# Performance work log

Hardware: AMD Instinct MI355X
Metric: run time of the kernel (lower is better)

The kernel has to match this reference:

```python
import jax, jax.numpy as jnp
import numpy as np

N_NODES = 50000
N_EDGES = 800000
IN_DIM = 128
HIDDEN = 64
HEADS = 4
N_GRAPHS = 256
NEG_SLOPE = 0.2  # PyG GATConv default


def gat_conv(x, src, dst, W, a_src, a_dst, b):
    """PyG-style GATConv (concat=True), eval mode (no dropout).
    x: [N, F_in]; src/dst: [E] (self-loops already included);
    W: [H*C, F_in]; a_src/a_dst: [H, C]; b: [H*C].
    """
    N = x.shape[0]
    H, C = a_src.shape
    h = (x @ W.T).reshape(N, H, C)                      # [N, H, C]
    alo = (h * a_src[None]).sum(-1)                     # [N, H]
    ahi = (h * a_dst[None]).sum(-1)                     # [N, H]
    e = jax.nn.leaky_relu(alo[src] + ahi[dst], NEG_SLOPE)  # [E, H]
    # segment softmax over destination neighborhoods
    m = jax.ops.segment_max(e, dst, num_segments=N)     # [N, H]
    ex = jnp.exp(e - m[dst])
    denom = jax.ops.segment_sum(ex, dst, num_segments=N)
    alpha = ex / (denom[dst] + 1e-16)                   # [E, H]
    out = jax.ops.segment_sum(h[src] * alpha[:, :, None], dst, num_segments=N)
    return out.reshape(N, H * C) + b


def setup_inputs() -> dict:
    key = jax.random.key(0)
    ks = jax.random.split(key, 24)
    p = lambda k, s: (jax.random.normal(k, s, jnp.float32) * 0.1)
    x = jax.random.normal(ks[0], (N_NODES, IN_DIM), jnp.float32)
    edge_index = jax.random.randint(ks[1], (2, N_EDGES), 0, N_NODES, jnp.int64 if jax.config.jax_enable_x64 else jnp.int32)
    batch_idx = jnp.sort(jax.random.randint(ks[2], (N_NODES,), 0, N_GRAPHS))
    HC = HIDDEN * HEADS
    return {
        "x": x, "edge_index": edge_index, "batch_idx": batch_idx,
        "W1": p(ks[3], (HC, IN_DIM)), "as1": p(ks[4], (HEADS, HIDDEN)), "ad1": p(ks[5], (HEADS, HIDDEN)), "b1": jnp.zeros((HC,), jnp.float32),
        "W2": p(ks[6], (HC, HC)), "as2": p(ks[7], (HEADS, HIDDEN)), "ad2": p(ks[8], (HEADS, HIDDEN)), "b2": jnp.zeros((HC,), jnp.float32),
        "W3": p(ks[9], (HIDDEN, HC)), "as3": p(ks[10], (1, HIDDEN)), "ad3": p(ks[11], (1, HIDDEN)), "b3": jnp.zeros((HIDDEN,), jnp.float32),
        "Wc1": p(ks[12], (HIDDEN, HIDDEN)), "bc1": jnp.zeros((HIDDEN,), jnp.float32),
        "Wc2": p(ks[13], (1, HIDDEN)), "bc2": jnp.zeros((1,), jnp.float32),
        "Wr1": p(ks[14], (HIDDEN, HIDDEN)), "br1": jnp.zeros((HIDDEN,), jnp.float32),
        "Wr2": p(ks[15], (1, HIDDEN)), "br2": jnp.zeros((1,), jnp.float32),
    }


def reference(x, edge_index, batch_idx, W1, as1, ad1, b1, W2, as2, ad2, b2, W3, as3, ad3, b3, Wc1, bc1, Wc2, bc2, Wr1, br1, Wr2, br2):
    N = x.shape[0]
    loops = jnp.arange(N, dtype=edge_index.dtype)
    src = jnp.concatenate([edge_index[0], loops])  # add_self_loops=True (PyG default)
    dst = jnp.concatenate([edge_index[1], loops])
    h = jax.nn.elu(gat_conv(x, src, dst, W1, as1, ad1, b1))
    h = jax.nn.elu(gat_conv(h, src, dst, W2, as2, ad2, b2))
    h = jax.nn.elu(gat_conv(h, src, dst, W3, as3, ad3, b3))  # [N, HIDDEN]
    # global mean pool over graphs
    cnt = jax.ops.segment_sum(jnp.ones((N,), h.dtype), batch_idx, num_segments=N_GRAPHS)
    g = jax.ops.segment_sum(h, batch_idx, num_segments=N_GRAPHS) / jnp.maximum(cnt, 1.0)[:, None]
    cls_logit = (jax.nn.relu(g @ Wc1.T + bc1) @ Wc2.T + bc2).reshape(-1)
    reg_pred = (jax.nn.relu(g @ Wr1.T + br1) @ Wr2.T + br2).reshape(-1)
    return (cls_logit, reg_pred)
```

## Files before the change

### kernel.cpp

```cpp
#include <hip/hip_runtime.h>

#define N_NODES 50000
#define N_EDGES 800000
#define EP_EDGES (N_EDGES + N_NODES)
#define N_GRAPHS 256
#define NBLK_SCAN ((N_NODES + 255) / 256)

typedef unsigned short u16;
typedef __attribute__((ext_vector_type(8))) short s8v;
typedef __attribute__((ext_vector_type(4))) float f4v;

__device__ __forceinline__ u16 fb(float f) {
  unsigned u = __float_as_uint(f);
  return (u16)((u + 0x7fffu + ((u >> 16) & 1u)) >> 16);
}
__device__ __forceinline__ float bfl(unsigned p) {
  return __uint_as_float(p << 16);
}
__device__ __forceinline__ float bfh(unsigned p) {
  return __uint_as_float(p & 0xffff0000u);
}
__device__ __forceinline__ float bff(u16 s) {
  return __uint_as_float(((unsigned)s) << 16);
}

#define W_N1 32768
#define W_N2 (W_N1 + 65536)
#define W_N3 (W_N2 + 16384)
__global__ void f2bw(const float* __restrict__ w1, const float* __restrict__ w2,
                     const float* __restrict__ w3, u16* __restrict__ w1b,
                     u16* __restrict__ w2b, u16* __restrict__ w3b) {
  int i = blockIdx.x * 256 + threadIdx.x;
  if (i < W_N1) w1b[i] = fb(w1[i]);
  else if (i < W_N2) w2b[i - W_N1] = fb(w2[i - W_N1]);
  else if (i < W_N3) w3b[i - W_N2] = fb(w3[i - W_N2]);
}

__device__ __forceinline__ void score_epilogue(
    f4v (&acc)[4][4], const float* __restrict__ a_src,
    const float* __restrict__ a_dst, float* __restrict__ alo,
    float* __restrict__ ahi, int m0, int n0, int wi, int wj, int quad, int fr,
    int M) {
  const int head = (n0 + wj) >> 6;
  float as[4], ad[4];
#pragma unroll
  for (int j = 0; j < 4; ++j) {
    int col = n0 + wj + j * 16 + fr;
    as[j] = a_src[col];
    ad[j] = a_dst[col];
  }
#pragma unroll
  for (int i = 0; i < 4; ++i) {
#pragma unroll
    for (int r = 0; r < 4; ++r) {
      float s = 0.f, d = 0.f;
#pragma unroll
      for (int j = 0; j < 4; ++j) {
        s += acc[i][j][r] * as[j];
        d += acc[i][j][r] * ad[j];
      }
#pragma unroll
      for (int off = 8; off; off >>= 1) {
        s += __shfl_xor(s, off, 64);
        d += __shfl_xor(d, off, 64);
      }
      int row = m0 + wi + i * 16 + quad * 4 + r;
      if (fr == 0 && row < M) {
        alo[row * 4 + head] = s;
        ahi[row * 4 + head] = d;
      }
    }
  }
}

__global__ __launch_bounds__(256) void gemm128(
    const u16* __restrict__ A, const u16* __restrict__ W,
    u16* __restrict__ C, const float* __restrict__ a_src,
    const float* __restrict__ a_dst, float* __restrict__ alo,
    float* __restrict__ ahi, int M, int Nout, int K) {
  __shared__ u16 As[128][40];
  __shared__ u16 Bs[128][40];
  const int t = threadIdx.x;
  const int m0 = blockIdx.y * 128, n0 = blockIdx.x * 128;
  const int rq = t >> 2, q = t & 3;
  const int w = t >> 6, lane = t & 63;
  const int wi = (w & 1) * 64, wj = (w >> 1) * 64;
  const int quad = lane >> 4, fr = lane & 15;

  f4v acc[4][4] = {};
  for (int k0 = 0; k0 < K; k0 += 32) {
    uint4 av[2], bv[2];
#pragma unroll
    for (int g = 0; g < 2; ++g) {
      int r = rq + g * 64;
      int m = m0 + r;
      av[g] = (m < M) ? *(const uint4*)&A[(size_t)m * K + k0 + q * 8]
                      : make_uint4(0, 0, 0, 0);
      bv[g] = *(const uint4*)&W[(size_t)(n0 + r) * K + k0 + q * 8];
    }
    __syncthreads();
#pragma unroll
    for (int g = 0; g < 2; ++g) {
      *(uint4*)&As[rq + g * 64][q * 8] = av[g];
      *(uint4*)&Bs[rq + g * 64][q * 8] = bv[g];
    }
    __syncthreads();
    s8v af[4], bf_[4];
#pragma unroll
    for (int i = 0; i < 4; ++i) {
      af[i] = *(const s8v*)&As[wi + i * 16 + fr][quad * 8];
      bf_[i] = *(const s8v*)&Bs[wj + i * 16 + fr][quad * 8];
    }
#pragma unroll
    for (int i = 0; i < 4; ++i)
#pragma unroll
      for (int j = 0; j < 4; ++j)
        acc[i][j] =
            __builtin_amdgcn_mfma_f32_16x16x32_bf16(af[i], bf_[j], acc[i][j], 0, 0, 0);
  }
#pragma unroll
  for (int i = 0; i < 4; ++i) {
    int rbase = m0 + wi + i * 16 + quad * 4;
#pragma unroll
    for (int j = 0; j < 4; ++j) {
      int col = n0 + wj + j * 16 + fr;
#pragma unroll
      for (int r = 0; r < 4; ++r) {
        int row = rbase + r;
        if (row < M) C[(size_t)row * Nout + col] = fb(acc[i][j][r]);
      }
    }
  }
  score_epilogue(acc, a_src, a_dst, alo, ahi, m0, n0, wi, wj, quad, fr, M);
}

__global__ __launch_bounds__(256) void gemm128_f32(
    const float* __restrict__ A, const u16* __restrict__ W,
    u16* __restrict__ C, const float* __restrict__ a_src,
    const float* __restrict__ a_dst, float* __restrict__ alo,
    float* __restrict__ ahi, int M, int Nout, int K) {
  __shared__ u16 As[128][40];
  __shared__ u16 Bs[128][40];
  const int t = threadIdx.x;
  const int m0 = blockIdx.y * 128, n0 = blockIdx.x * 128;
  const int rq = t >> 2, q = t & 3;
  const int w = t >> 6, lane = t & 63;
  const int wi = (w & 1) * 64, wj = (w >> 1) * 64;
  const int quad = lane >> 4, fr = lane & 15;

  f4v acc[4][4] = {};
  for (int k0 = 0; k0 < K; k0 += 32) {
    uint4 av[2], bv[2];
#pragma unroll
    for (int g = 0; g < 2; ++g) {
      int r = rq + g * 64;
      int m = m0 + r;
      if (m < M) {
        float4 f0 = *(const float4*)&A[(size_t)m * K + k0 + q * 8];
        float4 f1 = *(const float4*)&A[(size_t)m * K + k0 + q * 8 + 4];
        av[g].x = (unsigned)fb(f0.x) | ((unsigned)fb(f0.y) << 16);
        av[g].y = (unsigned)fb(f0.z) | ((unsigned)fb(f0.w) << 16);
        av[g].z = (unsigned)fb(f1.x) | ((unsigned)fb(f1.y) << 16);
        av[g].w = (unsigned)fb(f1.z) | ((unsigned)fb(f1.w) << 16);
      } else {
        av[g] = make_uint4(0, 0, 0, 0);
      }
      bv[g] = *(const uint4*)&W[(size_t)(n0 + r) * K + k0 + q * 8];
    }
    __syncthreads();
#pragma unroll
    for (int g = 0; g < 2; ++g) {
      *(uint4*)&As[rq + g * 64][q * 8] = av[g];
      *(uint4*)&Bs[rq + g * 64][q * 8] = bv[g];
    }
    __syncthreads();
    s8v af[4], bf_[4];
#pragma unroll
    for (int i = 0; i < 4; ++i) {
      af[i] = *(const s8v*)&As[wi + i * 16 + fr][quad * 8];
      bf_[i] = *(const s8v*)&Bs[wj + i * 16 + fr][quad * 8];
    }
#pragma unroll
    for (int i = 0; i < 4; ++i)
#pragma unroll
      for (int j = 0; j < 4; ++j)
        acc[i][j] =
            __builtin_amdgcn_mfma_f32_16x16x32_bf16(af[i], bf_[j], acc[i][j], 0, 0, 0);
  }
#pragma unroll
  for (int i = 0; i < 4; ++i) {
    int rbase = m0 + wi + i * 16 + quad * 4;
#pragma unroll
    for (int j = 0; j < 4; ++j) {
      int col = n0 + wj + j * 16 + fr;
#pragma unroll
      for (int r = 0; r < 4; ++r) {
        int row = rbase + r;
        if (row < M) C[(size_t)row * Nout + col] = fb(acc[i][j][r]);
      }
    }
  }
  score_epilogue(acc, a_src, a_dst, alo, ahi, m0, n0, wi, wj, quad, fr, M);
}

__global__ __launch_bounds__(256) void gemm_bf16(
    const u16* __restrict__ A, const u16* __restrict__ W,
    u16* __restrict__ C, int M, int Nout, int K) {
  __shared__ u16 As[64][40];
  __shared__ u16 Bs[64][40];
  const int t = threadIdx.x;
  const int m0 = blockIdx.y * 64, n0 = blockIdx.x * 64;
  const int r = t >> 2, c = t & 3;
  const int w = t >> 6, lane = t & 63;
  const int mi = (w & 1) * 32, ni = (w >> 1) * 32;
  const int quad = lane >> 4, fr = lane & 15;

  f4v c00{}, c01{}, c10{}, c11{};
  for (int k0 = 0; k0 < K; k0 += 32) {
    uint4 av = make_uint4(0, 0, 0, 0);
    int m = m0 + r;
    if (m < M) av = *(const uint4*)&A[(size_t)m * K + k0 + c * 8];
    uint4 bv = *(const uint4*)&W[(size_t)(n0 + r) * K + k0 + c * 8];
    __syncthreads();
    *(uint4*)&As[r][c * 8] = av;
    *(uint4*)&Bs[r][c * 8] = bv;
    __syncthreads();
    s8v a0 = *(const s8v*)&As[mi + fr][quad * 8];
    s8v a1 = *(const s8v*)&As[mi + 16 + fr][quad * 8];
    s8v b0 = *(const s8v*)&Bs[ni + fr][quad * 8];
    s8v b1 = *(const s8v*)&Bs[ni + 16 + fr][quad * 8];
    c00 = __builtin_amdgcn_mfma_f32_16x16x32_bf16(a0, b0, c00, 0, 0, 0);
    c01 = __builtin_amdgcn_mfma_f32_16x16x32_bf16(a0, b1, c01, 0, 0, 0);
    c10 = __builtin_amdgcn_mfma_f32_16x16x32_bf16(a1, b0, c10, 0, 0, 0);
    c11 = __builtin_amdgcn_mfma_f32_16x16x32_bf16(a1, b1, c11, 0, 0, 0);
  }
  const int col = n0 + ni + fr;
#pragma unroll
  for (int i = 0; i < 4; ++i) {
    int row = m0 + mi + quad * 4 + i;
    if (row < M) {
      C[(size_t)row * Nout + col] = fb(c00[i]);
      C[(size_t)row * Nout + col + 16] = fb(c01[i]);
    }
    int row2 = row + 16;
    if (row2 < M) {
      C[(size_t)row2 * Nout + col] = fb(c10[i]);
      C[(size_t)row2 * Nout + col + 16] = fb(c11[i]);
    }
  }
}

__global__ void k_hist(const int* __restrict__ ei, int* __restrict__ deg) {
  int e = blockIdx.x * 256 + threadIdx.x;
  if (e >= EP_EDGES) return;
  int d = (e < N_EDGES) ? ei[N_EDGES + e] : e - N_EDGES;
  atomicAdd(&deg[d], 1);
}

__global__ void k_scan_local(const int* __restrict__ deg,
                             int* __restrict__ rowstart,
                             int* __restrict__ bsum) {
  __shared__ int sh[256];
  const int tid = threadIdx.x;
  const int i = blockIdx.x * 256 + tid;
  int v = (i < N_NODES) ? deg[i] : 0;
  sh[tid] = v;
  __syncthreads();
  for (int off = 1; off < 256; off <<= 1) {
    int add = (tid >= off) ? sh[tid - off] : 0;
    __syncthreads();
    sh[tid] += add;
    __syncthreads();
  }
  if (i < N_NODES) rowstart[i] = sh[tid] - v;
  if (tid == 255) bsum[blockIdx.x] = sh[255];
}

__global__ void k_scan_bsum(int* __restrict__ bsum, int* __restrict__ boff) {
  __shared__ int sh[256];
  const int tid = threadIdx.x;
  int v = (tid < NBLK_SCAN) ? bsum[tid] : 0;
  sh[tid] = v;
  __syncthreads();
  for (int off = 1; off < 256; off <<= 1) {
    int add = (tid >= off) ? sh[tid - off] : 0;
    __syncthreads();
    sh[tid] += add;
    __syncthreads();
  }
  boff[tid] = sh[tid] - v;
}

__global__ void k_scan_add(int* __restrict__ rowstart,
                           const int* __restrict__ boff) {
  int i = blockIdx.x * 256 + threadIdx.x;
  if (i < N_NODES) rowstart[i] += boff[i >> 8];
  if (i == N_NODES) rowstart[N_NODES] = EP_EDGES;
}

__global__ void k_scatter(const int* __restrict__ ei,
                          const int* __restrict__ rowstart,
                          int* __restrict__ fill, int* __restrict__ esrc) {
  int e = blockIdx.x * 256 + threadIdx.x;
  if (e >= EP_EDGES) return;
  int s, d;
  if (e < N_EDGES) { s = ei[e]; d = ei[N_EDGES + e]; }
  else             { s = d = e - N_EDGES; }
  int pos = rowstart[d] + atomicAdd(&fill[d], 1);
  esrc[pos] = s;
}

__global__ __launch_bounds__(64) void agg4(
    const int* __restrict__ rowstart, const int* __restrict__ esrc,
    const u16* __restrict__ hbuf, const float* __restrict__ alo,
    const float* __restrict__ ahi, const float* __restrict__ bias,
    u16* __restrict__ feat) {
  const int d = blockIdx.x;
  const int lane = threadIdx.x;
  const int head = lane >> 4;
  const int c = lane * 4;
  const int s0 = rowstart[d], s1 = rowstart[d + 1];
  const float ah = ahi[d * 4 + head];

  float l = 0.f, o0 = 0.f, o1 = 0.f, o2 = 0.f, o3 = 0.f;
  for (int j = s0; j < s1; j += 8) {
    int ss[8];
    float wq[8];
#pragma unroll
    for (int q = 0; q < 8; ++q) {
      int jj = j + q;
      int sv = esrc[jj < EP_EDGES ? jj : EP_EDGES - 1];
      ss[q] = (jj < s1) ? sv : d;
    }
#pragma unroll
    for (int q = 0; q < 8; ++q) {
      float e = alo[ss[q] * 4 + head] + ah;
      e = e > 0.f ? e : 0.2f * e;
      wq[q] = (j + q < s1) ? __expf(e) : 0.f;
    }
    uint2 hv[8];
#pragma unroll
    for (int q = 0; q < 8; ++q)
      hv[q] = *(const uint2*)&hbuf[(size_t)ss[q] * 256 + c];
#pragma unroll
    for (int q = 0; q < 8; ++q) {
      l += wq[q];
      o0 += wq[q] * bfl(hv[q].x);
      o1 += wq[q] * bfh(hv[q].x);
      o2 += wq[q] * bfl(hv[q].y);
      o3 += wq[q] * bfh(hv[q].y);
    }
  }
  const float inv = 1.f / (l + 1e-16f);
  float4 bv = *(const float4*)&bias[c];
  float v0 = o0 * inv + bv.x, v1 = o1 * inv + bv.y;
  float v2 = o2 * inv + bv.z, v3 = o3 * inv + bv.w;
  v0 = v0 > 0.f ? v0 : __expf(v0) - 1.f;
  v1 = v1 > 0.f ? v1 : __expf(v1) - 1.f;
  v2 = v2 > 0.f ? v2 : __expf(v2) - 1.f;
  v3 = v3 > 0.f ? v3 : __expf(v3) - 1.f;
  uint2 pv;
  pv.x = (unsigned)fb(v0) | ((unsigned)fb(v1) << 16);
  pv.y = (unsigned)fb(v2) | ((unsigned)fb(v3) << 16);
  *(uint2*)&feat[(size_t)d * 256 + c] = pv;
}

__global__ __launch_bounds__(64) void agg1(
    const int* __restrict__ rowstart, const int* __restrict__ esrc,
    const u16* __restrict__ hbuf, const float* __restrict__ a_src,
    const float* __restrict__ a_dst, const float* __restrict__ bias,
    float* __restrict__ feat) {
  const int d = blockIdx.x;
  const int t = threadIdx.x;
  const int s0 = rowstart[d], s1 = rowstart[d + 1];
  const float as = a_src[t];

  float hd = bff(hbuf[(size_t)d * 64 + t]);
  float ah = hd * a_dst[t];
#pragma unroll
  for (int off = 32; off; off >>= 1) ah += __shfl_xor(ah, off, 64);

  float l = 0.f, o = 0.f;
  for (int j = s0; j < s1; j += 4) {
    int ss[4];
    u16 hv[4];
#pragma unroll
    for (int q = 0; q < 4; ++q) {
      int jj = j + q;
      int sv = esrc[jj < EP_EDGES ? jj : EP_EDGES - 1];
      ss[q] = (jj < s1) ? sv : d;
    }
#pragma unroll
    for (int q = 0; q < 4; ++q) hv[q] = hbuf[(size_t)ss[q] * 64 + t];
#pragma unroll
    for (int q = 0; q < 4; ++q) {
      float hq = bff(hv[q]);
      float al = hq * as;
#pragma unroll
      for (int off = 32; off; off >>= 1) al += __shfl_xor(al, off, 64);
      float e = al + ah;
      e = e > 0.f ? e : 0.2f * e;
      float w = (j + q < s1) ? __expf(e) : 0.f;
      l += w;
      o += w * hq;
    }
  }
  float v = o / (l + 1e-16f) + bias[t];
  feat[(size_t)d * 64 + t] = v > 0.f ? v : __expf(v) - 1.f;
}

__global__ __launch_bounds__(64) void poolheads(
    const float* __restrict__ feat, const int* __restrict__ batch,
    const float* __restrict__ Wc1, const float* __restrict__ bc1,
    const float* __restrict__ Wc2, const float* __restrict__ bc2,
    const float* __restrict__ Wr1, const float* __restrict__ br1,
    const float* __restrict__ Wr2, const float* __restrict__ br2,
    float* __restrict__ out) {
  const int gi = blockIdx.x, t = threadIdx.x;
  int l = 0, r = N_NODES;
  while (l < r) { int m = (l + r) >> 1; if (batch[m] < gi) l = m + 1; else r = m; }
  const int lo = l;
  r = N_NODES;
  while (l < r) { int m = (l + r) >> 1; if (batch[m] < gi + 1) l = m + 1; else r = m; }
  const int hi = l;

  float acc = 0.f;
  for (int n = lo; n < hi; ++n) acc += feat[(size_t)n * 64 + t];
  float cnt = (float)(hi - lo);
  cnt = cnt < 1.f ? 1.f : cnt;

  __shared__ float g[64];
  g[t] = acc / cnt;
  __syncthreads();
  float hc = bc1[t], hr = br1[t];
#pragma unroll 8
  for (int c = 0; c < 64; ++c) {
    float gv = g[c];
    hc += gv * Wc1[t * 64 + c];
    hr += gv * Wr1[t * 64 + c];
  }
  hc = fmaxf(hc, 0.f) * Wc2[t];
  hr = fmaxf(hr, 0.f) * Wr2[t];
#pragma unroll
  for (int off = 32; off; off >>= 1) {
    hc += __shfl_down(hc, off, 64);
    hr += __shfl_down(hr, off, 64);
  }
  if (t == 0) {
    out[gi] = hc + bc2[0];
    out[N_GRAPHS + gi] = hr + br2[0];
  }
}

extern "C" void kernel_launch(void* const* d_in, const int* in_sizes, int n_in,
                              void* d_out, int out_size, void* d_ws,
                              size_t ws_size, hipStream_t stream) {
  const float* x   = (const float*)d_in[0];
  const int* ei    = (const int*)d_in[1];
  const int* batch = (const int*)d_in[2];
  const float* W1  = (const float*)d_in[3];
  const float* as1 = (const float*)d_in[4];
  const float* ad1 = (const float*)d_in[5];
  const float* b1  = (const float*)d_in[6];
  const float* W2  = (const float*)d_in[7];
  const float* as2 = (const float*)d_in[8];
  const float* ad2 = (const float*)d_in[9];
  const float* b2  = (const float*)d_in[10];
  const float* W3  = (const float*)d_in[11];
  const float* as3 = (const float*)d_in[12];
  const float* ad3 = (const float*)d_in[13];
  const float* b3  = (const float*)d_in[14];
  const float* Wc1 = (const float*)d_in[15];
  const float* bc1 = (const float*)d_in[16];
  const float* Wc2 = (const float*)d_in[17];
  const float* bc2 = (const float*)d_in[18];
  const float* Wr1 = (const float*)d_in[19];
  const float* br1 = (const float*)d_in[20];
  const float* Wr2 = (const float*)d_in[21];
  const float* br2 = (const float*)d_in[22];
  float* out = (float*)d_out;

  float* ws = (float*)d_ws;
  u16* h_buf = (u16*)ws;
  float* p = ws + (size_t)N_NODES * 128;
  u16* featb = (u16*)p;
  p += (size_t)N_NODES * 128;
  u16* W1b = (u16*)p; p += 16384;
  u16* W2b = (u16*)p; p += 32768;
  u16* W3b = (u16*)p; p += 8192;
  float* feat3 = p;   p += (size_t)N_NODES * 64;
  float* alo   = p;   p += (size_t)N_NODES * 4;
  float* ahi   = p;   p += (size_t)N_NODES * 4;
  int* rowstart = (int*)p; p += (N_NODES + 4);
  int* esrc    = (int*)p;  p += EP_EDGES;
  float* bsc   = p;
  int* deg  = (int*)alo;
  int* fill = (int*)alo + N_NODES;
  int* bsum = (int*)bsc;
  int* boff = (int*)bsc + 256;

  hipMemsetAsync(deg, 0, (size_t)2 * N_NODES * 4, stream);
  const int eblk = (EP_EDGES + 255) / 256;
  k_hist<<<eblk, 256, 0, stream>>>(ei, deg);
  k_scan_local<<<NBLK_SCAN, 256, 0, stream>>>(deg, rowstart, bsum);
  k_scan_bsum<<<1, 256, 0, stream>>>(bsum, boff);
  k_scan_add<<<(N_NODES + 256) / 256, 256, 0, stream>>>(rowstart, boff);
  k_scatter<<<eblk, 256, 0, stream>>>(ei, rowstart, fill, esrc);

  f2bw<<<(W_N3 + 255) / 256, 256, 0, stream>>>(W1, W2, W3, W1b, W2b, W3b);

  const int MB128 = (N_NODES + 127) / 128;
  const int MB64 = (N_NODES + 63) / 64;
  gemm128_f32<<<dim3(2, MB128), 256, 0, stream>>>(x, W1b, h_buf, as1, ad1, alo,
                                                  ahi, N_NODES, 256, 128);
  agg4<<<N_NODES, 64, 0, stream>>>(rowstart, esrc, h_buf, alo, ahi, b1, featb);
  gemm128<<<dim3(2, MB128), 256, 0, stream>>>(featb, W2b, h_buf, as2, ad2, alo,
                                              ahi, N_NODES, 256, 256);
  agg4<<<N_NODES, 64, 0, stream>>>(rowstart, esrc, h_buf, alo, ahi, b2, featb);
  gemm_bf16<<<dim3(1, MB64), 256, 0, stream>>>(featb, W3b, h_buf, N_NODES, 64, 256);
  agg1<<<N_NODES, 64, 0, stream>>>(rowstart, esrc, h_buf, as3, ad3, b3, feat3);

  poolheads<<<N_GRAPHS, 64, 0, stream>>>(feat3, batch, Wc1, bc1, Wc2, bc2, Wr1,
                                         br1, Wr2, br2, out);
}
```

Baseline: 561.8 us.

## Merge CSR build into cooperative kernel and fuse layer-3 scores into GEMM

The separate memset, histogram, three scan kernels, scatter and weight-conversion launches are replaced by one cooperative kernel that separates its phases with grid-wide syncs. This removes several launches and their gaps. The layer-3 GEMM now also computes the per-node source and destination attention scores in its epilogue, so agg1 reads a precomputed alo per neighbour instead of doing a 64-lane shuffle reduction for every edge. The risks are the cost of grid syncs over only 256 resident blocks, and fewer threads doing the atomic histogram and scatter.

```diff
diff --git a/kernel.cpp b/kernel.cpp
--- a/kernel.cpp
+++ b/kernel.cpp
@@ -1,10 +1,13 @@
 #include <hip/hip_runtime.h>
+#include <hip/hip_cooperative_groups.h>
+
+namespace cg = cooperative_groups;
 
 #define N_NODES 50000
 #define N_EDGES 800000
 #define EP_EDGES (N_EDGES + N_NODES)
 #define N_GRAPHS 256
-#define NBLK_SCAN ((N_NODES + 255) / 256)
+#define COOP_BLOCKS 256
 
 typedef unsigned short u16;
 typedef __attribute__((ext_vector_type(8))) short s8v;
@@ -27,13 +30,67 @@
 #define W_N1 32768
 #define W_N2 (W_N1 + 65536)
 #define W_N3 (W_N2 + 16384)
-__global__ void f2bw(const float* __restrict__ w1, const float* __restrict__ w2,
-                     const float* __restrict__ w3, u16* __restrict__ w1b,
-                     u16* __restrict__ w2b, u16* __restrict__ w3b) {
-  int i = blockIdx.x * 256 + threadIdx.x;
-  if (i < W_N1) w1b[i] = fb(w1[i]);
-  else if (i < W_N2) w2b[i - W_N1] = fb(w2[i - W_N1]);
-  else if (i < W_N3) w3b[i - W_N2] = fb(w3[i - W_N2]);
+
+__global__ __launch_bounds__(256) void prep_coop(
+    const int* __restrict__ ei, int* __restrict__ deg, int* __restrict__ fill,
+    int* __restrict__ rowstart, int* __restrict__ bsum, int* __restrict__ boff,
+    int* __restrict__ esrc, const float* __restrict__ w1,
+    const float* __restrict__ w2, const float* __restrict__ w3,
+    u16* __restrict__ w1b, u16* __restrict__ w2b, u16* __restrict__ w3b) {
+  cg::grid_group grid = cg::this_grid();
+  const int tid = blockIdx.x * 256 + threadIdx.x;
+  const int nthr = COOP_BLOCKS * 256;
+  __shared__ int sh[256];
+
+  for (int i = tid; i < 2 * N_NODES; i += nthr) deg[i] = 0;
+  for (int i = tid; i < W_N3; i += nthr) {
+    if (i < W_N1) w1b[i] = fb(w1[i]);
+    else if (i < W_N2) w2b[i - W_N1] = fb(w2[i - W_N1]);
+    else w3b[i - W_N2] = fb(w3[i - W_N2]);
+  }
+  grid.sync();
+  for (int e = tid; e < EP_EDGES; e += nthr) {
+    int d = (e < N_EDGES) ? ei[N_EDGES + e] : e - N_EDGES;
+    atomicAdd(&deg[d], 1);
+  }
+  grid.sync();
+  {
+    int v = (tid < N_NODES) ? deg[tid] : 0;
+    sh[threadIdx.x] = v;
+    __syncthreads();
+    for (int off = 1; off < 256; off <<= 1) {
+      int add = (threadIdx.x >= off) ? sh[threadIdx.x - off] : 0;
+      __syncthreads();
+      sh[threadIdx.x] += add;
+      __syncthreads();
+    }
+    if (tid < N_NODES) rowstart[tid] = sh[threadIdx.x] - v;
+    if (threadIdx.x == 255) bsum[blockIdx.x] = sh[255];
+  }
+  grid.sync();
+  if (blockIdx.x == 0) {
+    int v = bsum[threadIdx.x];
+    sh[threadIdx.x] = v;
+    __syncthreads();
+    for (int off = 1; off < 256; off <<= 1) {
+      int add = (threadIdx.x >= off) ? sh[threadIdx.x - off] : 0;
+      __syncthreads();
+      sh[threadIdx.x] += add;
+      __syncthreads();
+    }
+    boff[threadIdx.x] = sh[threadIdx.x] - v;
+  }
+  grid.sync();
+  for (int i = tid; i < N_NODES; i += nthr) rowstart[i] += boff[i >> 8];
+  if (tid == 0) rowstart[N_NODES] = EP_EDGES;
+  grid.sync();
+  for (int e = tid; e < EP_EDGES; e += nthr) {
+    int s, d;
+    if (e < N_EDGES) { s = ei[e]; d = ei[N_EDGES + e]; }
+    else             { s = d = e - N_EDGES; }
+    int pos = rowstart[d] + atomicAdd(&fill[d], 1);
+    esrc[pos] = s;
+  }
 }
 
 __device__ __forceinline__ void score_epilogue(
@@ -203,11 +260,14 @@
   score_epilogue(acc, a_src, a_dst, alo, ahi, m0, n0, wi, wj, quad, fr, M);
 }
 
-__global__ __launch_bounds__(256) void gemm_bf16(
+__global__ __launch_bounds__(256) void gemm64_s(
     const u16* __restrict__ A, const u16* __restrict__ W,
-    u16* __restrict__ C, int M, int Nout, int K) {
+    u16* __restrict__ C, const float* __restrict__ a_src,
+    const float* __restrict__ a_dst, float* __restrict__ alo,
+    float* __restrict__ ahi, int M, int Nout, int K) {
   __shared__ u16 As[64][40];
   __shared__ u16 Bs[64][40];
+  __shared__ float sh_s[64][2], sh_d[64][2];
   const int t = threadIdx.x;
   const int m0 = blockIdx.y * 64, n0 = blockIdx.x * 64;
   const int r = t >> 2, c = t & 3;
@@ -248,66 +308,36 @@
       C[(size_t)row2 * Nout + col + 16] = fb(c11[i]);
     }
   }
-}
-
-__global__ void k_hist(const int* __restrict__ ei, int* __restrict__ deg) {
-  int e = blockIdx.x * 256 + threadIdx.x;
-  if (e >= EP_EDGES) return;
-  int d = (e < N_EDGES) ? ei[N_EDGES + e] : e - N_EDGES;
-  atomicAdd(&deg[d], 1);
-}
-
-__global__ void k_scan_local(const int* __restrict__ deg,
-                             int* __restrict__ rowstart,
-                             int* __restrict__ bsum) {
-  __shared__ int sh[256];
-  const int tid = threadIdx.x;
-  const int i = blockIdx.x * 256 + tid;
-  int v = (i < N_NODES) ? deg[i] : 0;
-  sh[tid] = v;
+  const float as_lo = a_src[ni + fr], as_hi = a_src[ni + 16 + fr];
+  const float ad_lo = a_dst[ni + fr], ad_hi = a_dst[ni + 16 + fr];
+#pragma unroll
+  for (int i = 0; i < 4; ++i) {
+    float s0 = c00[i] * as_lo + c01[i] * as_hi;
+    float d0 = c00[i] * ad_lo + c01[i] * ad_hi;
+    float s1 = c10[i] * as_lo + c11[i] * as_hi;
+    float d1 = c10[i] * ad_lo + c11[i] * ad_hi;
+#pragma unroll
+    for (int off = 8; off; off >>= 1) {
+      s0 += __shfl_xor(s0, off, 64);
+      d0 += __shfl_xor(d0, off, 64);
+      s1 += __shfl_xor(s1, off, 64);
+      d1 += __shfl_xor(d1, off, 64);
+    }
+    if (fr == 0) {
+      sh_s[mi + quad * 4 + i][ni >> 5] = s0;
+      sh_d[mi + quad * 4 + i][ni >> 5] = d0;
+      sh_s[mi + 16 + quad * 4 + i][ni >> 5] = s1;
+      sh_d[mi + 16 + quad * 4 + i][ni >> 5] = d1;
+    }
+  }
   __syncthreads();
-  for (int off = 1; off < 256; off <<= 1) {
-    int add = (tid >= off) ? sh[tid - off] : 0;
-    __syncthreads();
-    sh[tid] += add;
-    __syncthreads();
-  }
-  if (i < N_NODES) rowstart[i] = sh[tid] - v;
-  if (tid == 255) bsum[blockIdx.x] = sh[255];
-}
-
-__global__ void k_scan_bsum(int* __restrict__ bsum, int* __restrict__ boff) {
-  __shared__ int sh[256];
-  const int tid = threadIdx.x;
-  int v = (tid < NBLK_SCAN) ? bsum[tid] : 0;
-  sh[tid] = v;
-  __syncthreads();
-  for (int off = 1; off < 256; off <<= 1) {
-    int add = (tid >= off) ? sh[tid - off] : 0;
-    __syncthreads();
-    sh[tid] += add;
-    __syncthreads();
-  }
-  boff[tid] = sh[tid] - v;
-}
-
-__global__ void k_scan_add(int* __restrict__ rowstart,
-                           const int* __restrict__ boff) {
-  int i = blockIdx.x * 256 + threadIdx.x;
-  if (i < N_NODES) rowstart[i] += boff[i >> 8];
-  if (i == N_NODES) rowstart[N_NODES] = EP_EDGES;
-}
-
-__global__ void k_scatter(const int* __restrict__ ei,
-                          const int* __restrict__ rowstart,
-                          int* __restrict__ fill, int* __restrict__ esrc) {
-  int e = blockIdx.x * 256 + threadIdx.x;
-  if (e >= EP_EDGES) return;
-  int s, d;
-  if (e < N_EDGES) { s = ei[e]; d = ei[N_EDGES + e]; }
-  else             { s = d = e - N_EDGES; }
-  int pos = rowstart[d] + atomicAdd(&fill[d], 1);
-  esrc[pos] = s;
+  if (t < 64) {
+    int row = m0 + t;
+    if (row < M) {
+      alo[row] = sh_s[t][0] + sh_s[t][1];
+      ahi[row] = sh_d[t][0] + sh_d[t][1];
+    }
+  }
 }
 
 __global__ __launch_bounds__(64) void agg4(
@@ -367,23 +397,18 @@
 
 __global__ __launch_bounds__(64) void agg1(
     const int* __restrict__ rowstart, const int* __restrict__ esrc,
-    const u16* __restrict__ hbuf, const float* __restrict__ a_src,
-    const float* __restrict__ a_dst, const float* __restrict__ bias,
+    const u16* __restrict__ hbuf, const float* __restrict__ alo,
+    const float* __restrict__ ahi, const float* __restrict__ bias,
     float* __restrict__ feat) {
   const int d = blockIdx.x;
   const int t = threadIdx.x;
   const int s0 = rowstart[d], s1 = rowstart[d + 1];
-  const float as = a_src[t];
-
-  float hd = bff(hbuf[(size_t)d * 64 + t]);
-  float ah = hd * a_dst[t];
-#pragma unroll
-  for (int off = 32; off; off >>= 1) ah += __shfl_xor(ah, off, 64);
+  const float ah = ahi[d];
 
   float l = 0.f, o = 0.f;
   for (int j = s0; j < s1; j += 4) {
     int ss[4];
-    u16 hv[4];
+    float wq[4];
 #pragma unroll
     for (int q = 0; q < 4; ++q) {
       int jj = j + q;
@@ -391,18 +416,18 @@
       ss[q] = (jj < s1) ? sv : d;
     }
 #pragma unroll
+    for (int q = 0; q < 4; ++q) {
+      float e = alo[ss[q]] + ah;
+      e = e > 0.f ? e : 0.2f * e;
+      wq[q] = (j + q < s1) ? __expf(e) : 0.f;
+    }
+    u16 hv[4];
+#pragma unroll
     for (int q = 0; q < 4; ++q) hv[q] = hbuf[(size_t)ss[q] * 64 + t];
 #pragma unroll
     for (int q = 0; q < 4; ++q) {
-      float hq = bff(hv[q]);
-      float al = hq * as;
-#pragma unroll
-      for (int off = 32; off; off >>= 1) al += __shfl_xor(al, off, 64);
-      float e = al + ah;
-      e = e > 0.f ? e : 0.2f * e;
-      float w = (j + q < s1) ? __expf(e) : 0.f;
-      l += w;
-      o += w * hq;
+      l += wq[q];
+      o += wq[q] * bff(hv[q]);
     }
   }
   float v = o / (l + 1e-16f) + bias[t];
@@ -499,15 +524,14 @@
   int* bsum = (int*)bsc;
   int* boff = (int*)bsc + 256;
 
-  hipMemsetAsync(deg, 0, (size_t)2 * N_NODES * 4, stream);
-  const int eblk = (EP_EDGES + 255) / 256;
-  k_hist<<<eblk, 256, 0, stream>>>(ei, deg);
-  k_scan_local<<<NBLK_SCAN, 256, 0, stream>>>(deg, rowstart, bsum);
-  k_scan_bsum<<<1, 256, 0, stream>>>(bsum, boff);
-  k_scan_add<<<(N_NODES + 256) / 256, 256, 0, stream>>>(rowstart, boff);
-  k_scatter<<<eblk, 256, 0, stream>>>(ei, rowstart, fill, esrc);
-
-  f2bw<<<(W_N3 + 255) / 256, 256, 0, stream>>>(W1, W2, W3, W1b, W2b, W3b);
+  {
+    void* args[] = {(void*)&ei,  (void*)&deg,  (void*)&fill, (void*)&rowstart,
+                    (void*)&bsum, (void*)&boff, (void*)&esrc, (void*)&W1,
+                    (void*)&W2,   (void*)&W3,   (void*)&W1b,  (void*)&W2b,
+                    (void*)&W3b};
+    hipLaunchCooperativeKernel((const void*)prep_coop, dim3(COOP_BLOCKS),
+                               dim3(256), args, 0, stream);
+  }
 
   const int MB128 = (N_NODES + 127) / 128;
   const int MB64 = (N_NODES + 63) / 64;
@@ -517,8 +541,9 @@
   gemm128<<<dim3(2, MB128), 256, 0, stream>>>(featb, W2b, h_buf, as2, ad2, alo,
                                               ahi, N_NODES, 256, 256);
   agg4<<<N_NODES, 64, 0, stream>>>(rowstart, esrc, h_buf, alo, ahi, b2, featb);
-  gemm_bf16<<<dim3(1, MB64), 256, 0, stream>>>(featb, W3b, h_buf, N_NODES, 64, 256);
-  agg1<<<N_NODES, 64, 0, stream>>>(rowstart, esrc, h_buf, as3, ad3, b3, feat3);
+  gemm64_s<<<dim3(1, MB64), 256, 0, stream>>>(featb, W3b, h_buf, as3, ad3, alo,
+                                              ahi, N_NODES, 64, 256);
+  agg1<<<N_NODES, 64, 0, stream>>>(rowstart, esrc, h_buf, alo, ahi, b3, feat3);
 
   poolheads<<<N_GRAPHS, 64, 0, stream>>>(feat3, batch, Wc1, bc1, Wc2, bc2, Wr1,
                                          br1, Wr2, br2, out);
```

Result: slower. 695.6 us (+23.8%).
